# Performance work log

Hardware: AMD Instinct MI355X
Metric: run time of the kernel (lower is better)

## Reference

```python
import jax, jax.numpy as jnp
import numpy as np

N_NODES = 100000
N_EDGES = 1600000
DIN = 128
DH = 128
EPS = 1e-5


def _gcn_conv(x, src, dst, W, b, n):
    # x: [N, F_in] -> [N, F_out]; PyG GCNConv: transform, add self-loops,
    # symmetric normalization D^-1/2 (A+I) D^-1/2, scatter-add, + bias.
    h = x @ W.T                                        # [N, F_out]
    loops = jnp.arange(n, dtype=src.dtype)
    s = jnp.concatenate([src, loops])                  # [E+N]
    d = jnp.concatenate([dst, loops])                  # [E+N]
    w = jnp.ones(s.shape[0], dtype=x.dtype)
    deg = jax.ops.segment_sum(w, d, num_segments=n)    # [N]
    dinv = jnp.where(deg > 0, jax.lax.rsqrt(deg), 0.0)
    norm = dinv[s] * dinv[d]                           # [E+N]
    msg = h[s] * norm[:, None]                         # [E+N, F_out] (big buffer)
    out = jax.ops.segment_sum(msg, d, num_segments=n)  # [N, F_out]
    return out + b


def setup_inputs() -> dict:
    key = jax.random.key(0)
    ks = jax.random.split(key, 8)
    x = jax.random.normal(ks[0], (N_NODES, DIN), dtype=jnp.float32)
    edge_index = jax.random.randint(ks[1], (2, N_EDGES), 0, N_NODES, dtype=jnp.int32)
    sc = 1.0 / np.sqrt(DIN)
    return {
        "x": x,
        "edge_index": edge_index,
        "gamma": jnp.ones((DIN,), jnp.float32),
        "beta": jnp.zeros((DIN,), jnp.float32),
        "W1": jax.random.normal(ks[2], (DH, DIN), jnp.float32) * sc,
        "b1": jnp.zeros((DH,), jnp.float32),
        "W2": jax.random.normal(ks[3], (DH, DH), jnp.float32) * (1.0 / np.sqrt(DH)),
        "b2": jnp.zeros((DH,), jnp.float32),
        "Wc1": jax.random.normal(ks[4], (16, DH), jnp.float32) * (1.0 / np.sqrt(DH)),
        "bc1": jnp.zeros((16,), jnp.float32),
        "Wc2": jax.random.normal(ks[5], (2, 16), jnp.float32) * 0.25,
        "bc2": jnp.zeros((2,), jnp.float32),
    }


def reference(x, edge_index, gamma, beta, W1, b1, W2, b2, Wc1, bc1, Wc2, bc2):
    n = x.shape[0]
    src, dst = edge_index[0], edge_index[1]
    # BatchNorm1d (training mode: batch stats, biased variance)
    mu = jnp.mean(x, axis=0)
    var = jnp.mean((x - mu) ** 2, axis=0)
    xn = (x - mu) * jax.lax.rsqrt(var + EPS) * gamma + beta
    h = jax.nn.relu(_gcn_conv(xn, src, dst, W1, b1, n))
    h = jax.nn.relu(_gcn_conv(h, src, dst, W2, b2, n))
    h = jax.nn.relu(h @ Wc1.T + bc1)
    return h @ Wc2.T + bc2  # [N, 2]
```

## Files before the change

### kernel.cpp

```cpp
#include <hip/hip_runtime.h>
#include <hip/hip_fp16.h>

#define NFEAT 128
#define EPSV 1e-5f
#define BSH 9
#define BSZ 512
#define CHUNK 8192
#define CAP 12288

typedef _Float16 h8 __attribute__((ext_vector_type(8)));
typedef float f4 __attribute__((ext_vector_type(4)));

__global__ __launch_bounds__(256) void k_front(const float4* __restrict__ X4,
    float* __restrict__ part, int total4,
    const int* __restrict__ src, const int* __restrict__ dst,
    int* __restrict__ bnxt, int* __restrict__ packed, int E, int NB)
{
    __shared__ float4 ls[256], lq[256];
    __shared__ int hist[1024], base[1024];
    int t = threadIdx.x;

    if (blockIdx.x < 256) {
        int stride = 256 * 256;
        int i = blockIdx.x * 256 + t;
        float4 s = make_float4(0.f, 0.f, 0.f, 0.f);
        float4 q = make_float4(0.f, 0.f, 0.f, 0.f);
        for (; i + 3 * stride < total4; i += 4 * stride) {
            float4 a = X4[i], b = X4[i + stride], c = X4[i + 2 * stride], d = X4[i + 3 * stride];
            s.x += (a.x + b.x) + (c.x + d.x);
            s.y += (a.y + b.y) + (c.y + d.y);
            s.z += (a.z + b.z) + (c.z + d.z);
            s.w += (a.w + b.w) + (c.w + d.w);
            q.x += (a.x * a.x + b.x * b.x) + (c.x * c.x + d.x * d.x);
            q.y += (a.y * a.y + b.y * b.y) + (c.y * c.y + d.y * d.y);
            q.z += (a.z * a.z + b.z * b.z) + (c.z * c.z + d.z * d.z);
            q.w += (a.w * a.w + b.w * b.w) + (c.w * c.w + d.w * d.w);
        }
        for (; i < total4; i += stride) {
            float4 a = X4[i];
            s.x += a.x; s.y += a.y; s.z += a.z; s.w += a.w;
            q.x = fmaf(a.x, a.x, q.x); q.y = fmaf(a.y, a.y, q.y);
            q.z = fmaf(a.z, a.z, q.z); q.w = fmaf(a.w, a.w, q.w);
        }
        ls[t] = s; lq[t] = q;
        __syncthreads();
        #pragma unroll
        for (int off = 128; off >= 32; off >>= 1) {
            if (t < off) {
                float4 a = ls[t], b = ls[t + off];
                ls[t] = make_float4(a.x + b.x, a.y + b.y, a.z + b.z, a.w + b.w);
                float4 c = lq[t], d = lq[t + off];
                lq[t] = make_float4(c.x + d.x, c.y + d.y, c.z + d.z, c.w + d.w);
            }
            __syncthreads();
        }
        if (t < 32) {
            float4* p4 = (float4*)(part + blockIdx.x * 256);
            p4[t] = ls[t];
            p4[32 + t] = lq[t];
        }
    } else {
        int cb = blockIdx.x - 256;
        int c0 = cb * (CHUNK / 4);
        int c1 = min(E >> 2, c0 + CHUNK / 4);
        const int4* dst4 = (const int4*)dst;
        const int4* src4 = (const int4*)src;
        for (int i = t; i < NB; i += 256) hist[i] = 0;
        __syncthreads();
        for (int e = c0 + t; e < c1; e += 256) {
            int4 d = dst4[e];
            atomicAdd(&hist[d.x >> BSH], 1);
            atomicAdd(&hist[d.y >> BSH], 1);
            atomicAdd(&hist[d.z >> BSH], 1);
            atomicAdd(&hist[d.w >> BSH], 1);
        }
        __syncthreads();
        for (int i = t; i < NB; i += 256) {
            int h = hist[i];
            base[i] = h ? atomicAdd(&bnxt[i], h) : 0;
            hist[i] = 0;
        }
        __syncthreads();
        for (int e = c0 + t; e < c1; e += 256) {
            int4 d = dst4[e];
            int4 s = src4[e];
            int b, p;
            b = d.x >> BSH; p = base[b] + atomicAdd(&hist[b], 1); packed[b * CAP + p] = (s.x << BSH) | (d.x & (BSZ - 1));
            b = d.y >> BSH; p = base[b] + atomicAdd(&hist[b], 1); packed[b * CAP + p] = (s.y << BSH) | (d.y & (BSZ - 1));
            b = d.z >> BSH; p = base[b] + atomicAdd(&hist[b], 1); packed[b * CAP + p] = (s.z << BSH) | (d.z & (BSZ - 1));
            b = d.w >> BSH; p = base[b] + atomicAdd(&hist[b], 1); packed[b * CAP + p] = (s.w << BSH) | (d.w & (BSZ - 1));
        }
        if (cb == 0) {
            for (int e = (E & ~3) + t; e < E; e += 256) {
                int d = dst[e];
                int b = d >> BSH;
                int p = atomicAdd(&bnxt[b], 1);
                packed[b * CAP + p] = (src[e] << BSH) | (d & (BSZ - 1));
            }
        }
    }
}

__global__ __launch_bounds__(256) void k_stats2(const float* __restrict__ part,
    float* __restrict__ part2)
{
    int v = threadIdx.x;
    int b0 = blockIdx.x * 32;
    float s = 0.f;
    #pragma unroll 8
    for (int j = 0; j < 32; ++j) s += part[(b0 + j) * 256 + v];
    part2[blockIdx.x * 256 + v] = s;
}

__global__ __launch_bounds__(256) void k_foldW(const float* __restrict__ W1,
    const float* __restrict__ gamma, const float* __restrict__ beta,
    const float* __restrict__ part2, float invN,
    float* __restrict__ W1p, float* __restrict__ c1)
{
    int o = (blockIdx.x * 256 + threadIdx.x) >> 6;
    int l = threadIdx.x & 63;
    float part = 0.f;
    #pragma unroll
    for (int j = 0; j < 2; ++j) {
        int k = 2 * l + j;
        float sm = 0.f, sq = 0.f;
        #pragma unroll
        for (int b = 0; b < 8; ++b) {
            sm += part2[b * 256 + k];
            sq += part2[b * 256 + 128 + k];
        }
        float mu = sm * invN;
        float var = fmaf(-mu, mu, sq * invN);
        float sc = rsqrtf(var + EPSV) * gamma[k];
        float sh = fmaf(-mu, sc, beta[k]);
        float w = W1[o * NFEAT + k];
        W1p[o * NFEAT + k] = w * sc;
        part = fmaf(sh, w, part);
    }
    #pragma unroll
    for (int off = 32; off > 0; off >>= 1) part += __shfl_down(part, off);
    if (l == 0) c1[o] = part;
}

__global__ __launch_bounds__(256) void k_bdp(const int* __restrict__ packed,
    const int* __restrict__ bnxt,
    int* __restrict__ rp, float* __restrict__ dinv,
    int* __restrict__ csr, int N, int E, int NB)
{
    __shared__ int cnt[BSZ];
    __shared__ int ps[256];
    __shared__ int pb[256];
    int b = blockIdx.x, t = threadIdx.x;
    cnt[2 * t] = 0; cnt[2 * t + 1] = 0;
    int v = (t < NB) ? bnxt[t] : 0;
    pb[t] = v;
    __syncthreads();
    #pragma unroll
    for (int off = 1; off < 256; off <<= 1) {
        int u = pb[t];
        if (t >= off) u += pb[t - off];
        __syncthreads();
        pb[t] = u;
        __syncthreads();
    }
    int boffb = (b == 0) ? 0 : pb[b - 1];
    int ecnt = bnxt[b];
    const int* pk = packed + b * CAP;
    const int4* p4 = (const int4*)pk;
    int n4 = ecnt >> 2;
    for (int e = t; e < n4; e += 256) {
        int4 w = p4[e];
        atomicAdd(&cnt[w.x & (BSZ - 1)], 1);
        atomicAdd(&cnt[w.y & (BSZ - 1)], 1);
        atomicAdd(&cnt[w.z & (BSZ - 1)], 1);
        atomicAdd(&cnt[w.w & (BSZ - 1)], 1);
    }
    for (int e = (n4 << 2) + t; e < ecnt; e += 256)
        atomicAdd(&cnt[pk[e] & (BSZ - 1)], 1);
    __syncthreads();
    int v0 = cnt[2 * t], v1 = cnt[2 * t + 1];
    int ts = v0 + v1;
    ps[t] = ts;
    __syncthreads();
    #pragma unroll
    for (int off = 1; off < 256; off <<= 1) {
        int u = ps[t];
        if (t >= off) u += ps[t - off];
        __syncthreads();
        ps[t] = u;
        __syncthreads();
    }
    int gbase = boffb + ps[t] - ts;
    cnt[2 * t] = gbase;
    cnt[2 * t + 1] = gbase + v0;
    int nbase = b << BSH;
    if (nbase + 2 * t < N) {
        rp[nbase + 2 * t] = gbase;
        dinv[nbase + 2 * t] = rsqrtf((float)(v0 + 1));
    }
    if (nbase + 2 * t + 1 < N) {
        rp[nbase + 2 * t + 1] = gbase + v0;
        dinv[nbase + 2 * t + 1] = rsqrtf((float)(v1 + 1));
    }
    if (b == 0 && t == 0) rp[N] = E;
    __syncthreads();
    for (int e = t; e < n4; e += 256) {
        int4 w = p4[e];
        int p;
        p = atomicAdd(&cnt[w.x & (BSZ - 1)], 1); csr[p] = w.x >> BSH;
        p = atomicAdd(&cnt[w.y & (BSZ - 1)], 1); csr[p] = w.y >> BSH;
        p = atomicAdd(&cnt[w.z & (BSZ - 1)], 1); csr[p] = w.z >> BSH;
        p = atomicAdd(&cnt[w.w & (BSZ - 1)], 1); csr[p] = w.w >> BSH;
    }
    for (int e = (n4 << 2) + t; e < ecnt; e += 256) {
        int w = pk[e];
        int p = atomicAdd(&cnt[w & (BSZ - 1)], 1);
        csr[p] = w >> BSH;
    }
}

__global__ __launch_bounds__(256) void k_gemm_f32(const float4* __restrict__ X4,
    const float* __restrict__ W, const float* __restrict__ C,
    const float* __restrict__ dinv, _Float16* __restrict__ Y, int N)
{
    __shared__ _Float16 w16[NFEAT * 136];
    __shared__ _Float16 ost[4 * 16 * 136];
    const float4* W4 = (const float4*)W;
    for (int idx = threadIdx.x; idx < NFEAT * NFEAT / 4; idx += 256) {
        float4 w = W4[idx];
        int o = idx >> 5, k = (idx & 31) * 4;
        _Float16* d = &w16[o * 136 + k];
        d[0] = (_Float16)w.x; d[1] = (_Float16)w.y;
        d[2] = (_Float16)w.z; d[3] = (_Float16)w.w;
    }
    __syncthreads();

    const h8* Wv = (const h8*)w16;
    h8* Yv = (h8*)Y;
    int lane = threadIdx.x & 63;
    int lr = lane & 15;
    int lk = lane >> 4;
    _Float16* slab = ost + (threadIdx.x >> 6) * (16 * 136);
    h8* slabv = (h8*)slab;
    int wid = (blockIdx.x * blockDim.x + threadIdx.x) >> 6;
    int nw = (gridDim.x * blockDim.x) >> 6;
    int ntiles = N >> 4;

    for (int tile = wid; tile < ntiles; tile += nw) {
        int r0 = tile << 4;
        h8 a[4];
        #pragma unroll
        for (int kg = 0; kg < 4; ++kg) {
            long fi = (long)(r0 + lr) * 32 + (kg * 4 + lk) * 2;
            float4 u = X4[fi];
            float4 v = X4[fi + 1];
            a[kg][0] = (_Float16)u.x; a[kg][1] = (_Float16)u.y;
            a[kg][2] = (_Float16)u.z; a[kg][3] = (_Float16)u.w;
            a[kg][4] = (_Float16)v.x; a[kg][5] = (_Float16)v.y;
            a[kg][6] = (_Float16)v.z; a[kg][7] = (_Float16)v.w;
        }

        f4 acc[8];
        #pragma unroll
        for (int nt = 0; nt < 8; ++nt) acc[nt] = (f4)(0.f);
        #pragma unroll
        for (int nt = 0; nt < 8; ++nt) {
            int o = nt * 16 + lr;
            #pragma unroll
            for (int kg = 0; kg < 4; ++kg) {
                h8 b = Wv[o * 17 + kg * 4 + lk];
                acc[nt] = __builtin_amdgcn_mfma_f32_16x16x32_f16(a[kg], b, acc[nt], 0, 0, 0);
            }
        }

        int rbase = lk * 4;
        float dv0 = dinv[r0 + rbase + 0];
        float dv1 = dinv[r0 + rbase + 1];
        float dv2 = dinv[r0 + rbase + 2];
        float dv3 = dinv[r0 + rbase + 3];
        #pragma unroll
        for (int nt = 0; nt < 8; ++nt) {
            int c = nt * 16 + lr;
            float cb = C[c];
            slab[(rbase + 0) * 136 + c] = (_Float16)((acc[nt][0] + cb) * dv0);
            slab[(rbase + 1) * 136 + c] = (_Float16)((acc[nt][1] + cb) * dv1);
            slab[(rbase + 2) * 136 + c] = (_Float16)((acc[nt][2] + cb) * dv2);
            slab[(rbase + 3) * 136 + c] = (_Float16)((acc[nt][3] + cb) * dv3);
        }
        #pragma unroll
        for (int j = 0; j < 4; ++j) {
            int row = j * 4 + lk;
            Yv[(long)(r0 + row) * 16 + lr] = slabv[row * 17 + lr];
        }
    }
}

__global__ __launch_bounds__(256) void k_gemm_f16(const _Float16* __restrict__ X,
    const float* __restrict__ W, const float* __restrict__ dinv,
    _Float16* __restrict__ Y, int N)
{
    __shared__ _Float16 w16[NFEAT * 136];
    __shared__ _Float16 ost[4 * 16 * 136];
    const float4* W4 = (const float4*)W;
    for (int idx = threadIdx.x; idx < NFEAT * NFEAT / 4; idx += 256) {
        float4 w = W4[idx];
        int o = idx >> 5, k = (idx & 31) * 4;
        _Float16* d = &w16[o * 136 + k];
        d[0] = (_Float16)w.x; d[1] = (_Float16)w.y;
        d[2] = (_Float16)w.z; d[3] = (_Float16)w.w;
    }
    __syncthreads();

    const h8* Xv = (const h8*)X;
    const h8* Wv = (const h8*)w16;
    h8* Yv = (h8*)Y;
    int lane = threadIdx.x & 63;
    int lr = lane & 15;
    int lk = lane >> 4;
    _Float16* slab = ost + (threadIdx.x >> 6) * (16 * 136);
    h8* slabv = (h8*)slab;
    int wid = (blockIdx.x * blockDim.x + threadIdx.x) >> 6;
    int nw = (gridDim.x * blockDim.x) >> 6;
    int ntiles = N >> 4;

    for (int tile = wid; tile < ntiles; tile += nw) {
        int r0 = tile << 4;
        h8 a[4];
        #pragma unroll
        for (int kg = 0; kg < 4; ++kg)
            a[kg] = Xv[(long)(r0 + lr) * 16 + kg * 4 + lk];

        f4 acc[8];
        #pragma unroll
        for (int nt = 0; nt < 8; ++nt) acc[nt] = (f4)(0.f);
        #pragma unroll
        for (int nt = 0; nt < 8; ++nt) {
            int o = nt * 16 + lr;
            #pragma unroll
            for (int kg = 0; kg < 4; ++kg) {
                h8 b = Wv[o * 17 + kg * 4 + lk];
                acc[nt] = __builtin_amdgcn_mfma_f32_16x16x32_f16(a[kg], b, acc[nt], 0, 0, 0);
            }
        }

        int rbase = lk * 4;
        float dv0 = dinv[r0 + rbase + 0];
        float dv1 = dinv[r0 + rbase + 1];
        float dv2 = dinv[r0 + rbase + 2];
        float dv3 = dinv[r0 + rbase + 3];
        #pragma unroll
        for (int nt = 0; nt < 8; ++nt) {
            int c = nt * 16 + lr;
            slab[(rbase + 0) * 136 + c] = (_Float16)(acc[nt][0] * dv0);
            slab[(rbase + 1) * 136 + c] = (_Float16)(acc[nt][1] * dv1);
            slab[(rbase + 2) * 136 + c] = (_Float16)(acc[nt][2] * dv2);
            slab[(rbase + 3) * 136 + c] = (_Float16)(acc[nt][3] * dv3);
        }
        #pragma unroll
        for (int j = 0; j < 4; ++j) {
            int row = j * 4 + lk;
            Yv[(long)(r0 + row) * 16 + lr] = slabv[row * 17 + lr];
        }
    }
}

__global__ __launch_bounds__(256) void k_agg(const unsigned int* __restrict__ TT,
    const int* __restrict__ rp, const int* __restrict__ csr,
    const float* __restrict__ dinv, const float* __restrict__ bias,
    unsigned int* __restrict__ OUT, int N)
{
    int wid = (blockIdx.x * 256 + threadIdx.x) >> 6;
    if (wid >= N) return;
    int lane = threadIdx.x & 63;
    unsigned int sv = TT[wid * 64 + lane];
    float2 acc = __half22float2(*(const __half2*)&sv);
    int e = rp[wid], e1 = rp[wid + 1];
    for (; e + 16 <= e1; e += 16) {
        int si[16];
        #pragma unroll
        for (int j = 0; j < 16; ++j) si[j] = csr[e + j];
        unsigned int v[16];
        #pragma unroll
        for (int j = 0; j < 16; ++j) v[j] = TT[si[j] * 64 + lane];
        float ax = 0.f, ay = 0.f;
        #pragma unroll
        for (int j = 0; j < 16; ++j) {
            float2 f = __half22float2(*(const __half2*)&v[j]);
            ax += f.x; ay += f.y;
        }
        acc.x += ax; acc.y += ay;
    }
    for (; e + 8 <= e1; e += 8) {
        int s0 = csr[e + 0], s1 = csr[e + 1], s2 = csr[e + 2], s3 = csr[e + 3];
        int s4 = csr[e + 4], s5 = csr[e + 5], s6 = csr[e + 6], s7 = csr[e + 7];
        unsigned int v0 = TT[s0 * 64 + lane];
        unsigned int v1 = TT[s1 * 64 + lane];
        unsigned int v2 = TT[s2 * 64 + lane];
        unsigned int v3 = TT[s3 * 64 + lane];
        unsigned int v4 = TT[s4 * 64 + lane];
        unsigned int v5 = TT[s5 * 64 + lane];
        unsigned int v6 = TT[s6 * 64 + lane];
        unsigned int v7 = TT[s7 * 64 + lane];
        float2 f0 = __half22float2(*(const __half2*)&v0);
        float2 f1 = __half22float2(*(const __half2*)&v1);
        float2 f2 = __half22float2(*(const __half2*)&v2);
        float2 f3 = __half22float2(*(const __half2*)&v3);
        float2 f4_ = __half22float2(*(const __half2*)&v4);
        float2 f5 = __half22float2(*(const __half2*)&v5);
        float2 f6 = __half22float2(*(const __half2*)&v6);
        float2 f7 = __half22float2(*(const __half2*)&v7);
        acc.x += ((f0.x + f1.x) + (f2.x + f3.x)) + ((f4_.x + f5.x) + (f6.x + f7.x));
        acc.y += ((f0.y + f1.y) + (f2.y + f3.y)) + ((f4_.y + f5.y) + (f6.y + f7.y));
    }
    for (; e < e1; ++e) {
        int s = csr[e];
        unsigned int v = TT[s * 64 + lane];
        float2 f = __half22float2(*(const __half2*)&v);
        acc.x += f.x; acc.y += f.y;
    }
    float dv = dinv[wid];
    float ox = fmaxf(fmaf(acc.x, dv, bias[lane * 2 + 0]), 0.f);
    float oy = fmaxf(fmaf(acc.y, dv, bias[lane * 2 + 1]), 0.f);
    __half2 o2 = __floats2half2_rn(ox, oy);
    OUT[wid * 64 + lane] = *(unsigned int*)&o2;
}

__global__ __launch_bounds__(256) void k_head(const __half* __restrict__ H,
    const float* __restrict__ Wc1, const float* __restrict__ bc1,
    const float* __restrict__ Wc2, const float* __restrict__ bc2,
    float* __restrict__ OUT, int N)
{
    __shared__ float w1[16][132];
    __shared__ float hs[16][132];
    __shared__ float h16[16][17];
    const float4* Wc14 = (const float4*)Wc1;
    for (int idx = threadIdx.x; idx < 16 * NFEAT / 4; idx += 256) {
        float4 w = Wc14[idx];
        int o = idx >> 5, k = (idx & 31) * 4;
        w1[o][k] = w.x; w1[o][k + 1] = w.y; w1[o][k + 2] = w.z; w1[o][k + 3] = w.w;
    }
    const uint4* Hu4 = (const uint4*)H;
    int ntiles = (N + 15) >> 4;
    for (int tile = blockIdx.x; tile < ntiles; tile += gridDim.x) {
        int row0 = tile << 4;
        __syncthreads();
        {
            int r = threadIdx.x >> 4, p = threadIdx.x & 15;
            int row = row0 + r;
            uint4 v = (row < N) ? Hu4[(long)row * 16 + p] : make_uint4(0, 0, 0, 0);
            float2 f0 = __half22float2(*(const __half2*)&v.x);
            float2 f1 = __half22float2(*(const __half2*)&v.y);
            float2 f2 = __half22float2(*(const __half2*)&v.z);
            float2 f3 = __half22float2(*(const __half2*)&v.w);
            int c = p * 8;
            hs[r][c + 0] = f0.x; hs[r][c + 1] = f0.y;
            hs[r][c + 2] = f1.x; hs[r][c + 3] = f1.y;
            hs[r][c + 4] = f2.x; hs[r][c + 5] = f2.y;
            hs[r][c + 6] = f3.x; hs[r][c + 7] = f3.y;
        }
        __syncthreads();
        int r = threadIdx.x >> 4, o = threadIdx.x & 15;
        float acc = 0.f;
        #pragma unroll 8
        for (int k = 0; k < NFEAT; ++k) acc = fmaf(hs[r][k], w1[o][k], acc);
        h16[r][o] = fmaxf(acc + bc1[o], 0.f);
        __syncthreads();
        if (threadIdx.x < 32) {
            int rr = threadIdx.x >> 1, j = threadIdx.x & 1;
            float a = bc2[j];
            #pragma unroll
            for (int o2 = 0; o2 < 16; ++o2) a = fmaf(h16[rr][o2], Wc2[j * 16 + o2], a);
            int row = row0 + rr;
            if (row < N) OUT[(long)row * 2 + j] = a;
        }
        __syncthreads();
    }
}

extern "C" void kernel_launch(void* const* d_in, const int* in_sizes, int n_in,
                              void* d_out, int out_size, void* d_ws, size_t ws_size,
                              hipStream_t stream) {
    const float* x     = (const float*)d_in[0];
    const int*   ei    = (const int*)d_in[1];
    const float* gamma = (const float*)d_in[2];
    const float* beta  = (const float*)d_in[3];
    const float* W1    = (const float*)d_in[4];
    const float* b1    = (const float*)d_in[5];
    const float* W2    = (const float*)d_in[6];
    const float* b2    = (const float*)d_in[7];
    const float* Wc1   = (const float*)d_in[8];
    const float* bc1   = (const float*)d_in[9];
    const float* Wc2   = (const float*)d_in[10];
    const float* bc2   = (const float*)d_in[11];

    int N = in_sizes[0] / NFEAT;
    int E = in_sizes[1] / 2;
    const int* srcI = ei;
    const int* dstI = ei + E;
    int NB = (N + BSZ - 1) >> BSH;

    char* ws = (char*)d_ws;
    size_t off = 0;
    auto alloc = [&](size_t bytes) {
        void* p = ws + off;
        off += bytes;
        off = (off + 511) & ~(size_t)511;
        return p;
    };
    __half* bufA  = (__half*)alloc((size_t)N * NFEAT * 2);
    __half* bufB  = (__half*)alloc((size_t)N * NFEAT * 2);
    float* part   = (float*)alloc(256 * 256 * 4);
    float* part2  = (float*)alloc(8 * 256 * 4);
    float* W1p    = (float*)alloc(NFEAT * NFEAT * 4);
    float* c1     = (float*)alloc(NFEAT * 4);
    int*   rp     = (int*)alloc((size_t)(N + 1) * 4);
    float* dinv   = (float*)alloc((size_t)N * 4);
    int*   csr    = (int*)alloc((size_t)E * 4);
    int*   packed = (int*)alloc((size_t)NB * CAP * 4);
    int*   bnxt   = (int*)alloc((size_t)(NB + 1) * 4);
    (void)ws_size;

    hipMemsetAsync(bnxt, 0, (size_t)(NB + 1) * 4, stream);

    int total4 = (int)((long)N * NFEAT / 4);
    int nchunk = (E + CHUNK - 1) / CHUNK;
    int naggb = (N + 3) / 4;

    k_front<<<256 + nchunk, 256, 0, stream>>>((const float4*)x, part, total4,
                                              srcI, dstI, bnxt, packed, E, NB);
    k_stats2<<<8, 256, 0, stream>>>(part, part2);
    k_foldW<<<32, 256, 0, stream>>>(W1, gamma, beta, part2, 1.0f / (float)N, W1p, c1);
    k_bdp<<<NB, 256, 0, stream>>>(packed, bnxt, rp, dinv, csr, N, E, NB);

    k_gemm_f32<<<512, 256, 0, stream>>>((const float4*)x, W1p, c1, dinv, (_Float16*)bufB, N);
    k_agg<<<naggb, 256, 0, stream>>>((const unsigned int*)bufB, rp, csr, dinv, b1, (unsigned int*)bufA, N);
    k_gemm_f16<<<512, 256, 0, stream>>>((const _Float16*)bufA, W2, dinv, (_Float16*)bufB, N);
    k_agg<<<naggb, 256, 0, stream>>>((const unsigned int*)bufB, rp, csr, dinv, b2, (unsigned int*)bufA, N);
    k_head<<<2048, 256, 0, stream>>>(bufA, Wc1, bc1, Wc2, bc2, (float*)d_out, N);
}
```

Measured before the change: 250.1 us.

## Fuse CSR build with first GEMM and move dinv scaling into aggregation

The first GEMM no longer scales its output by dinv, so it can run in one launch alongside the CSR/degree construction blocks. The layer-1 aggregation instead multiplies each gathered neighbour row by its source dinv, loaded per edge. The stats2 reduction kernel is removed and foldW now reduces all 256 partials itself. Together this cuts the launch count and removes the dependency of GEMM1 on the CSR build, at the cost of extra random dinv loads per edge in layer-1 aggregation and a longer serial reduction in foldW.

```diff
diff --git a/kernel.cpp b/kernel.cpp
--- a/kernel.cpp
+++ b/kernel.cpp
@@ -101,33 +101,22 @@
     }
 }
 
-__global__ __launch_bounds__(256) void k_stats2(const float* __restrict__ part,
-    float* __restrict__ part2)
-{
-    int v = threadIdx.x;
-    int b0 = blockIdx.x * 32;
-    float s = 0.f;
-    #pragma unroll 8
-    for (int j = 0; j < 32; ++j) s += part[(b0 + j) * 256 + v];
-    part2[blockIdx.x * 256 + v] = s;
-}
-
 __global__ __launch_bounds__(256) void k_foldW(const float* __restrict__ W1,
     const float* __restrict__ gamma, const float* __restrict__ beta,
-    const float* __restrict__ part2, float invN,
+    const float* __restrict__ part, float invN,
     float* __restrict__ W1p, float* __restrict__ c1)
 {
     int o = (blockIdx.x * 256 + threadIdx.x) >> 6;
     int l = threadIdx.x & 63;
-    float part = 0.f;
+    float acc = 0.f;
     #pragma unroll
     for (int j = 0; j < 2; ++j) {
         int k = 2 * l + j;
         float sm = 0.f, sq = 0.f;
-        #pragma unroll
-        for (int b = 0; b < 8; ++b) {
-            sm += part2[b * 256 + k];
-            sq += part2[b * 256 + 128 + k];
+        #pragma unroll 8
+        for (int b = 0; b < 256; ++b) {
+            sm += part[b * 256 + k];
+            sq += part[b * 256 + 128 + k];
         }
         float mu = sm * invN;
         float var = fmaf(-mu, mu, sq * invN);
@@ -135,162 +124,155 @@
         float sh = fmaf(-mu, sc, beta[k]);
         float w = W1[o * NFEAT + k];
         W1p[o * NFEAT + k] = w * sc;
-        part = fmaf(sh, w, part);
+        acc = fmaf(sh, w, acc);
     }
     #pragma unroll
-    for (int off = 32; off > 0; off >>= 1) part += __shfl_down(part, off);
-    if (l == 0) c1[o] = part;
-}
-
-__global__ __launch_bounds__(256) void k_bdp(const int* __restrict__ packed,
-    const int* __restrict__ bnxt,
-    int* __restrict__ rp, float* __restrict__ dinv,
-    int* __restrict__ csr, int N, int E, int NB)
+    for (int off = 32; off > 0; off >>= 1) acc += __shfl_down(acc, off);
+    if (l == 0) c1[o] = acc;
+}
+
+__global__ __launch_bounds__(256) void k_mid(const float4* __restrict__ X4,
+    const float* __restrict__ W, const float* __restrict__ C,
+    _Float16* __restrict__ Y, int N,
+    const int* __restrict__ packed, const int* __restrict__ bnxt,
+    int* __restrict__ rp, float* __restrict__ dinv, int* __restrict__ csr,
+    int E, int NB)
 {
+    __shared__ _Float16 w16[NFEAT * 136];
+    __shared__ _Float16 ost[4 * 16 * 136];
     __shared__ int cnt[BSZ];
     __shared__ int ps[256];
     __shared__ int pb[256];
-    int b = blockIdx.x, t = threadIdx.x;
-    cnt[2 * t] = 0; cnt[2 * t + 1] = 0;
-    int v = (t < NB) ? bnxt[t] : 0;
-    pb[t] = v;
-    __syncthreads();
-    #pragma unroll
-    for (int off = 1; off < 256; off <<= 1) {
-        int u = pb[t];
-        if (t >= off) u += pb[t - off];
-        __syncthreads();
-        pb[t] = u;
-        __syncthreads();
-    }
-    int boffb = (b == 0) ? 0 : pb[b - 1];
-    int ecnt = bnxt[b];
-    const int* pk = packed + b * CAP;
-    const int4* p4 = (const int4*)pk;
-    int n4 = ecnt >> 2;
-    for (int e = t; e < n4; e += 256) {
-        int4 w = p4[e];
-        atomicAdd(&cnt[w.x & (BSZ - 1)], 1);
-        atomicAdd(&cnt[w.y & (BSZ - 1)], 1);
-        atomicAdd(&cnt[w.z & (BSZ - 1)], 1);
-        atomicAdd(&cnt[w.w & (BSZ - 1)], 1);
-    }
-    for (int e = (n4 << 2) + t; e < ecnt; e += 256)
-        atomicAdd(&cnt[pk[e] & (BSZ - 1)], 1);
-    __syncthreads();
-    int v0 = cnt[2 * t], v1 = cnt[2 * t + 1];
-    int ts = v0 + v1;
-    ps[t] = ts;
-    __syncthreads();
-    #pragma unroll
-    for (int off = 1; off < 256; off <<= 1) {
-        int u = ps[t];
-        if (t >= off) u += ps[t - off];
-        __syncthreads();
-        ps[t] = u;
-        __syncthreads();
-    }
-    int gbase = boffb + ps[t] - ts;
-    cnt[2 * t] = gbase;
-    cnt[2 * t + 1] = gbase + v0;
-    int nbase = b << BSH;
-    if (nbase + 2 * t < N) {
-        rp[nbase + 2 * t] = gbase;
-        dinv[nbase + 2 * t] = rsqrtf((float)(v0 + 1));
-    }
-    if (nbase + 2 * t + 1 < N) {
-        rp[nbase + 2 * t + 1] = gbase + v0;
-        dinv[nbase + 2 * t + 1] = rsqrtf((float)(v1 + 1));
-    }
-    if (b == 0 && t == 0) rp[N] = E;
-    __syncthreads();
-    for (int e = t; e < n4; e += 256) {
-        int4 w = p4[e];
-        int p;
-        p = atomicAdd(&cnt[w.x & (BSZ - 1)], 1); csr[p] = w.x >> BSH;
-        p = atomicAdd(&cnt[w.y & (BSZ - 1)], 1); csr[p] = w.y >> BSH;
-        p = atomicAdd(&cnt[w.z & (BSZ - 1)], 1); csr[p] = w.z >> BSH;
-        p = atomicAdd(&cnt[w.w & (BSZ - 1)], 1); csr[p] = w.w >> BSH;
-    }
-    for (int e = (n4 << 2) + t; e < ecnt; e += 256) {
-        int w = pk[e];
-        int p = atomicAdd(&cnt[w & (BSZ - 1)], 1);
-        csr[p] = w >> BSH;
-    }
-}
-
-__global__ __launch_bounds__(256) void k_gemm_f32(const float4* __restrict__ X4,
-    const float* __restrict__ W, const float* __restrict__ C,
-    const float* __restrict__ dinv, _Float16* __restrict__ Y, int N)
-{
-    __shared__ _Float16 w16[NFEAT * 136];
-    __shared__ _Float16 ost[4 * 16 * 136];
-    const float4* W4 = (const float4*)W;
-    for (int idx = threadIdx.x; idx < NFEAT * NFEAT / 4; idx += 256) {
-        float4 w = W4[idx];
-        int o = idx >> 5, k = (idx & 31) * 4;
-        _Float16* d = &w16[o * 136 + k];
-        d[0] = (_Float16)w.x; d[1] = (_Float16)w.y;
-        d[2] = (_Float16)w.z; d[3] = (_Float16)w.w;
-    }
-    __syncthreads();
-
-    const h8* Wv = (const h8*)w16;
-    h8* Yv = (h8*)Y;
-    int lane = threadIdx.x & 63;
-    int lr = lane & 15;
-    int lk = lane >> 4;
-    _Float16* slab = ost + (threadIdx.x >> 6) * (16 * 136);
-    h8* slabv = (h8*)slab;
-    int wid = (blockIdx.x * blockDim.x + threadIdx.x) >> 6;
-    int nw = (gridDim.x * blockDim.x) >> 6;
-    int ntiles = N >> 4;
-
-    for (int tile = wid; tile < ntiles; tile += nw) {
-        int r0 = tile << 4;
-        h8 a[4];
-        #pragma unroll
-        for (int kg = 0; kg < 4; ++kg) {
-            long fi = (long)(r0 + lr) * 32 + (kg * 4 + lk) * 2;
-            float4 u = X4[fi];
-            float4 v = X4[fi + 1];
-            a[kg][0] = (_Float16)u.x; a[kg][1] = (_Float16)u.y;
-            a[kg][2] = (_Float16)u.z; a[kg][3] = (_Float16)u.w;
-            a[kg][4] = (_Float16)v.x; a[kg][5] = (_Float16)v.y;
-            a[kg][6] = (_Float16)v.z; a[kg][7] = (_Float16)v.w;
-        }
-
-        f4 acc[8];
-        #pragma unroll
-        for (int nt = 0; nt < 8; ++nt) acc[nt] = (f4)(0.f);
-        #pragma unroll
-        for (int nt = 0; nt < 8; ++nt) {
-            int o = nt * 16 + lr;
+    int t = threadIdx.x;
+
+    if (blockIdx.x < 512) {
+        const float4* W4 = (const float4*)W;
+        for (int idx = t; idx < NFEAT * NFEAT / 4; idx += 256) {
+            float4 w = W4[idx];
+            int o = idx >> 5, k = (idx & 31) * 4;
+            _Float16* d = &w16[o * 136 + k];
+            d[0] = (_Float16)w.x; d[1] = (_Float16)w.y;
+            d[2] = (_Float16)w.z; d[3] = (_Float16)w.w;
+        }
+        __syncthreads();
+        const h8* Wv = (const h8*)w16;
+        h8* Yv = (h8*)Y;
+        int lane = t & 63;
+        int lr = lane & 15;
+        int lk = lane >> 4;
+        _Float16* slab = ost + (t >> 6) * (16 * 136);
+        h8* slabv = (h8*)slab;
+        int wid = (blockIdx.x * 256 + t) >> 6;
+        int nw = (512 * 256) >> 6;
+        int ntiles = N >> 4;
+        for (int tile = wid; tile < ntiles; tile += nw) {
+            int r0 = tile << 4;
+            h8 a[4];
             #pragma unroll
             for (int kg = 0; kg < 4; ++kg) {
-                h8 b = Wv[o * 17 + kg * 4 + lk];
-                acc[nt] = __builtin_amdgcn_mfma_f32_16x16x32_f16(a[kg], b, acc[nt], 0, 0, 0);
-            }
-        }
-
-        int rbase = lk * 4;
-        float dv0 = dinv[r0 + rbase + 0];
-        float dv1 = dinv[r0 + rbase + 1];
-        float dv2 = dinv[r0 + rbase + 2];
-        float dv3 = dinv[r0 + rbase + 3];
-        #pragma unroll
-        for (int nt = 0; nt < 8; ++nt) {
-            int c = nt * 16 + lr;
-            float cb = C[c];
-            slab[(rbase + 0) * 136 + c] = (_Float16)((acc[nt][0] + cb) * dv0);
-            slab[(rbase + 1) * 136 + c] = (_Float16)((acc[nt][1] + cb) * dv1);
-            slab[(rbase + 2) * 136 + c] = (_Float16)((acc[nt][2] + cb) * dv2);
-            slab[(rbase + 3) * 136 + c] = (_Float16)((acc[nt][3] + cb) * dv3);
-        }
-        #pragma unroll
-        for (int j = 0; j < 4; ++j) {
-            int row = j * 4 + lk;
-            Yv[(long)(r0 + row) * 16 + lr] = slabv[row * 17 + lr];
+                long fi = (long)(r0 + lr) * 32 + (kg * 4 + lk) * 2;
+                float4 u = X4[fi];
+                float4 v = X4[fi + 1];
+                a[kg][0] = (_Float16)u.x; a[kg][1] = (_Float16)u.y;
+                a[kg][2] = (_Float16)u.z; a[kg][3] = (_Float16)u.w;
+                a[kg][4] = (_Float16)v.x; a[kg][5] = (_Float16)v.y;
+                a[kg][6] = (_Float16)v.z; a[kg][7] = (_Float16)v.w;
+            }
+            f4 acc[8];
+            #pragma unroll
+            for (int nt = 0; nt < 8; ++nt) acc[nt] = (f4)(0.f);
+            #pragma unroll
+            for (int nt = 0; nt < 8; ++nt) {
+                int o = nt * 16 + lr;
+                #pragma unroll
+                for (int kg = 0; kg < 4; ++kg) {
+                    h8 b = Wv[o * 17 + kg * 4 + lk];
+                    acc[nt] = __builtin_amdgcn_mfma_f32_16x16x32_f16(a[kg], b, acc[nt], 0, 0, 0);
+                }
+            }
+            int rbase = lk * 4;
+            #pragma unroll
+            for (int nt = 0; nt < 8; ++nt) {
+                int c = nt * 16 + lr;
+                float cb = C[c];
+                slab[(rbase + 0) * 136 + c] = (_Float16)(acc[nt][0] + cb);
+                slab[(rbase + 1) * 136 + c] = (_Float16)(acc[nt][1] + cb);
+                slab[(rbase + 2) * 136 + c] = (_Float16)(acc[nt][2] + cb);
+                slab[(rbase + 3) * 136 + c] = (_Float16)(acc[nt][3] + cb);
+            }
+            #pragma unroll
+            for (int j = 0; j < 4; ++j) {
+                int row = j * 4 + lk;
+                Yv[(long)(r0 + row) * 16 + lr] = slabv[row * 17 + lr];
+            }
+        }
+    } else {
+        int b = blockIdx.x - 512;
+        cnt[2 * t] = 0; cnt[2 * t + 1] = 0;
+        int v = (t < NB) ? bnxt[t] : 0;
+        pb[t] = v;
+        __syncthreads();
+        #pragma unroll
+        for (int off = 1; off < 256; off <<= 1) {
+            int u = pb[t];
+            if (t >= off) u += pb[t - off];
+            __syncthreads();
+            pb[t] = u;
+            __syncthreads();
+        }
+        int boffb = (b == 0) ? 0 : pb[b - 1];
+        int ecnt = bnxt[b];
+        const int* pk = packed + b * CAP;
+        const int4* p4 = (const int4*)pk;
+        int n4 = ecnt >> 2;
+        for (int e = t; e < n4; e += 256) {
+            int4 w = p4[e];
+            atomicAdd(&cnt[w.x & (BSZ - 1)], 1);
+            atomicAdd(&cnt[w.y & (BSZ - 1)], 1);
+            atomicAdd(&cnt[w.z & (BSZ - 1)], 1);
+            atomicAdd(&cnt[w.w & (BSZ - 1)], 1);
+        }
+        for (int e = (n4 << 2) + t; e < ecnt; e += 256)
+            atomicAdd(&cnt[pk[e] & (BSZ - 1)], 1);
+        __syncthreads();
+        int v0 = cnt[2 * t], v1 = cnt[2 * t + 1];
+        int ts = v0 + v1;
+        ps[t] = ts;
+        __syncthreads();
+        #pragma unroll
+        for (int off = 1; off < 256; off <<= 1) {
+            int u = ps[t];
+            if (t >= off) u += ps[t - off];
+            __syncthreads();
+            ps[t] = u;
+            __syncthreads();
+        }
+        int gbase = boffb + ps[t] - ts;
+        cnt[2 * t] = gbase;
+        cnt[2 * t + 1] = gbase + v0;
+        int nbase = b << BSH;
+        if (nbase + 2 * t < N) {
+            rp[nbase + 2 * t] = gbase;
+            dinv[nbase + 2 * t] = rsqrtf((float)(v0 + 1));
+        }
+        if (nbase + 2 * t + 1 < N) {
+            rp[nbase + 2 * t + 1] = gbase + v0;
+            dinv[nbase + 2 * t + 1] = rsqrtf((float)(v1 + 1));
+        }
+        if (b == 0 && t == 0) rp[N] = E;
+        __syncthreads();
+        for (int e = t; e < n4; e += 256) {
+            int4 w = p4[e];
+            int p;
+            p = atomicAdd(&cnt[w.x & (BSZ - 1)], 1); csr[p] = w.x >> BSH;
+            p = atomicAdd(&cnt[w.y & (BSZ - 1)], 1); csr[p] = w.y >> BSH;
+            p = atomicAdd(&cnt[w.z & (BSZ - 1)], 1); csr[p] = w.z >> BSH;
+            p = atomicAdd(&cnt[w.w & (BSZ - 1)], 1); csr[p] = w.w >> BSH;
+        }
+        for (int e = (n4 << 2) + t; e < ecnt; e += 256) {
+            int w = pk[e];
+            int p = atomicAdd(&cnt[w & (BSZ - 1)], 1);
+            csr[p] = w >> BSH;
         }
     }
 }
@@ -364,6 +346,7 @@
     }
 }
 
+template<int SRCDINV>
 __global__ __launch_bounds__(256) void k_agg(const unsigned int* __restrict__ TT,
     const int* __restrict__ rp, const int* __restrict__ csr,
     const float* __restrict__ dinv, const float* __restrict__ bias,
@@ -372,8 +355,12 @@
     int wid = (blockIdx.x * 256 + threadIdx.x) >> 6;
     if (wid >= N) return;
     int lane = threadIdx.x & 63;
+    float dvw = dinv[wid];
     unsigned int sv = TT[wid * 64 + lane];
-    float2 acc = __half22float2(*(const __half2*)&sv);
+    float2 sf = __half22float2(*(const __half2*)&sv);
+    float2 acc;
+    if (SRCDINV) { acc.x = sf.x * dvw; acc.y = sf.y * dvw; }
+    else         { acc = sf; }
     int e = rp[wid], e1 = rp[wid + 1];
     for (; e + 16 <= e1; e += 16) {
         int si[16];
@@ -382,45 +369,54 @@
         unsigned int v[16];
         #pragma unroll
         for (int j = 0; j < 16; ++j) v[j] = TT[si[j] * 64 + lane];
+        float dv16[16];
+        if (SRCDINV) {
+            #pragma unroll
+            for (int j = 0; j < 16; ++j) dv16[j] = dinv[si[j]];
+        }
         float ax = 0.f, ay = 0.f;
         #pragma unroll
         for (int j = 0; j < 16; ++j) {
             float2 f = __half22float2(*(const __half2*)&v[j]);
-            ax += f.x; ay += f.y;
+            if (SRCDINV) { ax = fmaf(f.x, dv16[j], ax); ay = fmaf(f.y, dv16[j], ay); }
+            else         { ax += f.x; ay += f.y; }
         }
         acc.x += ax; acc.y += ay;
     }
     for (; e + 8 <= e1; e += 8) {
-        int s0 = csr[e + 0], s1 = csr[e + 1], s2 = csr[e + 2], s3 = csr[e + 3];
-        int s4 = csr[e + 4], s5 = csr[e + 5], s6 = csr[e + 6], s7 = csr[e + 7];
-        unsigned int v0 = TT[s0 * 64 + lane];
-        unsigned int v1 = TT[s1 * 64 + lane];
-        unsigned int v2 = TT[s2 * 64 + lane];
-        unsigned int v3 = TT[s3 * 64 + lane];
-        unsigned int v4 = TT[s4 * 64 + lane];
-        unsigned int v5 = TT[s5 * 64 + lane];
-        unsigned int v6 = TT[s6 * 64 + lane];
-        unsigned int v7 = TT[s7 * 64 + lane];
-        float2 f0 = __half22float2(*(const __half2*)&v0);
-        float2 f1 = __half22float2(*(const __half2*)&v1);
-        float2 f2 = __half22float2(*(const __half2*)&v2);
-        float2 f3 = __half22float2(*(const __half2*)&v3);
-        float2 f4_ = __half22float2(*(const __half2*)&v4);
-        float2 f5 = __half22float2(*(const __half2*)&v5);
-        float2 f6 = __half22float2(*(const __half2*)&v6);
-        float2 f7 = __half22float2(*(const __half2*)&v7);
-        acc.x += ((f0.x + f1.x) + (f2.x + f3.x)) + ((f4_.x + f5.x) + (f6.x + f7.x));
-        acc.y += ((f0.y + f1.y) + (f2.y + f3.y)) + ((f4_.y + f5.y) + (f6.y + f7.y));
+        int si[8];
+        #pragma unroll
+        for (int j = 0; j < 8; ++j) si[j] = csr[e + j];
+        unsigned int v[8];
+        #pragma unroll
+        for (int j = 0; j < 8; ++j) v[j] = TT[si[j] * 64 + lane];
+        float dv8[8];
+        if (SRCDINV) {
+            #pragma unroll
+            for (int j = 0; j < 8; ++j) dv8[j] = dinv[si[j]];
+        }
+        float ax = 0.f, ay = 0.f;
+        #pragma unroll
+        for (int j = 0; j < 8; ++j) {
+            float2 f = __half22float2(*(const __half2*)&v[j]);
+            if (SRCDINV) { ax = fmaf(f.x, dv8[j], ax); ay = fmaf(f.y, dv8[j], ay); }
+            else         { ax += f.x; ay += f.y; }
+        }
+        acc.x += ax; acc.y += ay;
     }
     for (; e < e1; ++e) {
         int s = csr[e];
         unsigned int v = TT[s * 64 + lane];
         float2 f = __half22float2(*(const __half2*)&v);
-        acc.x += f.x; acc.y += f.y;
-    }
-    float dv = dinv[wid];
-    float ox = fmaxf(fmaf(acc.x, dv, bias[lane * 2 + 0]), 0.f);
-    float oy = fmaxf(fmaf(acc.y, dv, bias[lane * 2 + 1]), 0.f);
+        if (SRCDINV) {
+            float dv = dinv[s];
+            acc.x = fmaf(f.x, dv, acc.x); acc.y = fmaf(f.y, dv, acc.y);
+        } else {
+            acc.x += f.x; acc.y += f.y;
+        }
+    }
+    float ox = fmaxf(fmaf(acc.x, dvw, bias[lane * 2 + 0]), 0.f);
+    float oy = fmaxf(fmaf(acc.y, dvw, bias[lane * 2 + 1]), 0.f);
     __half2 o2 = __floats2half2_rn(ox, oy);
     OUT[wid * 64 + lane] = *(unsigned int*)&o2;
 }
@@ -510,7 +506,6 @@
     __half* bufA  = (__half*)alloc((size_t)N * NFEAT * 2);
     __half* bufB  = (__half*)alloc((size_t)N * NFEAT * 2);
     float* part   = (float*)alloc(256 * 256 * 4);
-    float* part2  = (float*)alloc(8 * 256 * 4);
     float* W1p    = (float*)alloc(NFEAT * NFEAT * 4);
     float* c1     = (float*)alloc(NFEAT * 4);
     int*   rp     = (int*)alloc((size_t)(N + 1) * 4);
@@ -528,13 +523,12 @@
 
     k_front<<<256 + nchunk, 256, 0, stream>>>((const float4*)x, part, total4,
                                               srcI, dstI, bnxt, packed, E, NB);
-    k_stats2<<<8, 256, 0, stream>>>(part, part2);
-    k_foldW<<<32, 256, 0, stream>>>(W1, gamma, beta, part2, 1.0f / (float)N, W1p, c1);
-    k_bdp<<<NB, 256, 0, stream>>>(packed, bnxt, rp, dinv, csr, N, E, NB);
-
-    k_gemm_f32<<<512, 256, 0, stream>>>((const float4*)x, W1p, c1, dinv, (_Float16*)bufB, N);
-    k_agg<<<naggb, 256, 0, stream>>>((const unsigned int*)bufB, rp, csr, dinv, b1, (unsigned int*)bufA, N);
+    k_foldW<<<32, 256, 0, stream>>>(W1, gamma, beta, part, 1.0f / (float)N, W1p, c1);
+    k_mid<<<512 + NB, 256, 0, stream>>>((const float4*)x, W1p, c1,
+                                        (_Float16*)bufB, N,
+                                        packed, bnxt, rp, dinv, csr, E, NB);
+    k_agg<1><<<naggb, 256, 0, stream>>>((const unsigned int*)bufB, rp, csr, dinv, b1, (unsigned int*)bufA, N);
     k_gemm_f16<<<512, 256, 0, stream>>>((const _Float16*)bufA, W2, dinv, (_Float16*)bufB, N);
-    k_agg<<<naggb, 256, 0, stream>>>((const unsigned int*)bufB, rp, csr, dinv, b2, (unsigned int*)bufA, N);
+    k_agg<0><<<naggb, 256, 0, stream>>>((const unsigned int*)bufB, rp, csr, dinv, b2, (unsigned int*)bufA, N);
     k_head<<<2048, 256, 0, stream>>>(bufA, Wc1, bc1, Wc2, bc2, (float*)d_out, N);
 }
```

Measured after the change: 289.8 us. +15.9%, slower.
